# Optimization experiments

Measured on AMD Instinct MI355X. Metric: run time of the kernel, lower is better.

Reference implementation:

```python
import jax, jax.numpy as jnp
import numpy as np
from jax import lax

EPS = 1e-5
DN = ('NCHW', 'OIHW', 'NCHW')


def _bn(x, gamma, beta, mean, var):
    # eval-mode BatchNorm2d over channel dim (axis=1)
    s = gamma / jnp.sqrt(var + EPS)
    return x * s[None, :, None, None] + (beta - mean * s)[None, :, None, None]


def setup_inputs() -> dict:
    key = jax.random.key(0)
    ks = jax.random.split(key, 12)
    B, Cin, C, H, W, NC = 128, 2048, 512, 14, 14, 200
    return {
        'feature': jax.random.normal(ks[0], (B, Cin, H, W), jnp.float32),
        'w_reduce': jax.random.normal(ks[1], (C, Cin, 1, 1), jnp.float32) * 0.02,
        'b_reduce': jax.random.normal(ks[2], (C,), jnp.float32) * 0.02,
        'bn1_gamma': jnp.ones((C,), jnp.float32),
        'bn1_beta': jnp.zeros((C,), jnp.float32),
        'bn1_mean': jax.random.normal(ks[3], (C,), jnp.float32) * 0.02,
        'bn1_var': jax.random.uniform(ks[4], (C,), jnp.float32),
        'w3': jax.random.normal(ks[5], (C, C, 3, 3), jnp.float32) * 0.02,
        'b3': jax.random.normal(ks[6], (C,), jnp.float32) * 0.02,
        'bn2_gamma': jnp.ones((C,), jnp.float32),
        'bn2_beta': jnp.zeros((C,), jnp.float32),
        'bn2_mean': jax.random.normal(ks[7], (C,), jnp.float32) * 0.02,
        'bn2_var': jax.random.uniform(ks[8], (C,), jnp.float32),
        'fc1_w': jax.random.normal(ks[9], (NC, C), jnp.float32) * 0.02,
        'fc1_b': jnp.zeros((NC,), jnp.float32),
        'fc2_w': jax.random.normal(ks[10], (NC, NC), jnp.float32) * 0.02,
        'fc2_b': jnp.zeros((NC,), jnp.float32),
    }


def reference(feature, w_reduce, b_reduce, bn1_gamma, bn1_beta, bn1_mean, bn1_var,
              w3, b3, bn2_gamma, bn2_beta, bn2_mean, bn2_var,
              fc1_w, fc1_b, fc2_w, fc2_b):
    B, _, H, W = feature.shape
    C = w_reduce.shape[0]  # 512
    # reduce: 1x1 conv + BN + ReLU
    f = lax.conv_general_dilated(feature, w_reduce, (1, 1), 'VALID', dimension_numbers=DN)
    f = f + b_reduce[None, :, None, None]
    f = jax.nn.relu(_bn(f, bn1_gamma, bn1_beta, bn1_mean, bn1_var))
    x = f.reshape(B, C, H * W)  # [B, 512, 196]
    # channel affinity + softmax(-xxt) over last dim (= the per-row loop)
    xxt = jnp.einsum('bcn,bdn->bcd', x, x)  # [B, 512, 512]
    a = jax.nn.softmax(-xxt, axis=2)
    y = jnp.einsum('bcd,bdn->bcn', a, x).reshape(B, C, H, W)
    # conv3: 3x3 conv + BN + ReLU + global avg pool
    z = lax.conv_general_dilated(y, w3, (1, 1), 'SAME', dimension_numbers=DN)
    z = z + b3[None, :, None, None]
    z = jax.nn.relu(_bn(z, bn2_gamma, bn2_beta, bn2_mean, bn2_var))
    z = jnp.mean(z, axis=(2, 3))  # [B, 512]
    # fc_channel: Linear -> ReLU -> Linear
    h = jax.nn.relu(z @ fc1_w.T + fc1_b)
    sf = h @ fc2_w.T + fc2_b
    return sf
```

## Files before the change

### kernel.cpp

```cpp
#include <hip/hip_runtime.h>

typedef __attribute__((ext_vector_type(8))) short bf16x8;
typedef __attribute__((ext_vector_type(4))) float f32x4;
typedef __attribute__((ext_vector_type(4))) short short4v;

__device__ __forceinline__ unsigned short f2bf(float x){
  unsigned u = __float_as_uint(x);
  return (unsigned short)((u + 0x7FFFu + ((u>>16)&1u)) >> 16);
}
__device__ __forceinline__ float bf2f(unsigned short b){
  return __uint_as_float(((unsigned)b)<<16);
}

typedef const __attribute__((address_space(1))) void* gas_t;
typedef __attribute__((address_space(3))) void* las_t;
__device__ __forceinline__ void gl16(const void* g, void* l){
  __builtin_amdgcn_global_load_lds((gas_t)g, (las_t)l, 16, 0, 0);
}

static constexpr size_t O_FHI  = 0;
static constexpr size_t O_FLO  = 102760448;
static constexpr size_t O_XHI  = 205520896;
static constexpr size_t O_XLO  = 239075328;
static constexpr size_t O_XT   = 272629760;
static constexpr size_t O_AMAT = 301989888;
static constexpr size_t O_WH   = 369098752;
static constexpr size_t O_WL   = 371195904;
static constexpr size_t O_W3B  = 373293056;
static constexpr size_t O_PAR  = 378011648;
static constexpr size_t O_FC1T = 378019840;
static constexpr size_t O_FC2T = 378429440;
static constexpr size_t O_ZBAR = 378589440;

__global__ void k_params(const float* br, const float* g1, const float* be1, const float* m1, const float* v1,
                         const float* b3, const float* g2, const float* be2, const float* m2, const float* v2,
                         float* par){
  int c = blockIdx.x*256 + threadIdx.x;
  if (c >= 512) return;
  float s1 = g1[c] * rsqrtf(v1[c] + 1e-5f);
  par[c] = s1;
  par[512+c] = (br[c]-m1[c])*s1 + be1[c];
  float s2 = g2[c] * rsqrtf(v2[c] + 1e-5f);
  par[1024+c] = s2;
  par[1536+c] = (b3[c]-m2[c])*s2 + be2[c];
}

__global__ void k_wrhl(const float* wr, unsigned short* wh, unsigned short* wl){
  int k = blockIdx.x*256 + threadIdx.x;
  int c = blockIdx.y;
  float v = wr[(size_t)c*2048 + k];
  unsigned short h = f2bf(v);
  wh[(size_t)c*2048 + k] = h;
  wl[(size_t)c*2048 + k] = f2bf(v - bf2f(h));
}

__global__ void k_w3c(const float* w3, unsigned short* w3c){
  int k = blockIdx.x*256 + threadIdx.x;
  int co = blockIdx.y;
  int ci0b = k/576; int r2 = k - ci0b*576;
  int tap = r2>>6;  int cio = r2&63;
  w3c[(((size_t)ci0b*9 + tap)*512 + co)*64 + cio] =
      f2bf(w3[((size_t)co*512 + ci0b*64 + cio)*9 + tap]);
}

__global__ void k_fc1t(const float* w, float* wt){
  int i = blockIdx.x*256 + threadIdx.x;
  int k = i/200, j = i - k*200;
  wt[i] = w[j*512 + k];
}
__global__ void k_fc2t(const float* w, float* wt){
  int i = blockIdx.x*256 + threadIdx.x;
  if (i >= 200*200) return;
  int k = i/200, j = i - k*200;
  wt[i] = w[j*200 + k];
}

__global__ __launch_bounds__(256) void k_zeropad(unsigned short* xhi, unsigned short* xlo){
  int rr = blockIdx.x*256 + threadIdx.x;
  float4 z = {0.f,0.f,0.f,0.f};
  float4* a = (float4*)(xhi + (size_t)rr*256 + 192);
  float4* b = (float4*)(xlo + (size_t)rr*256 + 192);
  #pragma unroll
  for (int j=0;j<8;++j){ a[j] = z; b[j] = z; }
}

__global__ __launch_bounds__(256) void k_zeroyb(unsigned short* ypad){
  int tile = blockIdx.x;
  int r = threadIdx.x;
  if (r >= 256) return;
  int hi = r>>4, lo = r&15;
  bool pad = (hi==0)||(hi==15)||(lo==0)||(lo==15);
  if (!pad) return;
  float4 z = {0.f,0.f,0.f,0.f};
  float4* p = (float4*)(ypad + ((size_t)tile*256 + r)*64);
  #pragma unroll
  for (int j=0;j<8;++j) p[j] = z;
}

__global__ __launch_bounds__(256) void k_featT(const float* __restrict__ feat,
        unsigned short* __restrict__ fhi, unsigned short* __restrict__ flo){
  __shared__ float tile[64][33];
  int b = blockIdx.z;
  int ci0 = blockIdx.y*64, p0 = blockIdx.x*32;
  int t = threadIdx.x;
  int j = t & 31, i0 = t >> 5;
  for (int rep=0; rep<8; ++rep){
    int i = rep*8 + i0;
    int p = p0 + j;
    tile[i][j] = (p<196) ? feat[((size_t)b*2048 + ci0 + i)*196 + p] : 0.f;
  }
  __syncthreads();
  int ii = t & 63, jj0 = t >> 6;
  for (int rep=0; rep<8; ++rep){
    int jj = rep*4 + jj0;
    int p = p0 + jj;
    if (p < 196){
      float v = tile[ii][jj];
      unsigned short h = f2bf(v);
      size_t o = ((size_t)b*196 + p)*2048 + ci0 + ii;
      fhi[o] = h;
      flo[o] = f2bf(v - bf2f(h));
    }
  }
}

__global__ __launch_bounds__(256) void k_conv1(
    const unsigned short* __restrict__ fhi, const unsigned short* __restrict__ flo,
    const unsigned short* __restrict__ wh,  const unsigned short* __restrict__ wl,
    const float* __restrict__ par,
    unsigned short* __restrict__ xhi, unsigned short* __restrict__ xlo,
    unsigned short* __restrict__ xT){
  __shared__ char lds[32768];
  char* Als = lds; char* Bls = lds + 16384;
  int lin = blockIdx.x;
  int sz  = (lin&7)*98 + (lin>>3);
  int mt = sz&3;
  int gt = sz>>2;
  int c0 = mt*128;
  size_t g0 = (size_t)gt*128;
  int t = threadIdx.x, lane = t&63, wid = t>>6, wm = wid&1, wn = wid>>1;
  int fq = lane>>4, fr = lane&15;
  f32x4 acc[4][4] = {};
  for (int it=0; it<96; ++it){
    int seg = it>>5, kk0 = (it&31)*64;
    const unsigned short* As = (seg<2) ? wh : wl;
    const unsigned short* Bs = (seg==1) ? flo : fhi;
    __syncthreads();
    #pragma unroll
    for (int r=0;r<4;++r){
      int L = r*256 + t;
      int row = L>>3, cs = ((L&7)^(row&7))*8;
      gl16(As + (size_t)(c0+row)*2048 + kk0 + cs, Als + L*16);
      gl16(Bs + (g0+row)*2048 + kk0 + cs, Bls + L*16);
    }
    __syncthreads();
    #pragma unroll
    for (int ks=0; ks<2; ++ks){
      int kb = ks*64 + fq*16;
      bf16x8 af[4];
      #pragma unroll
      for (int m=0;m<4;++m){
        int row = wm*64 + m*16 + fr;
        af[m] = *(const bf16x8*)(Als + row*128 + (kb ^ ((row&7)<<4)));
      }
      #pragma unroll
      for (int n=0;n<4;++n){
        int row = wn*64 + n*16 + fr;
        bf16x8 bff = *(const bf16x8*)(Bls + row*128 + (kb ^ ((row&7)<<4)));
        #pragma unroll
        for (int m=0;m<4;++m)
          acc[m][n] = __builtin_amdgcn_mfma_f32_16x16x32_bf16(af[m], bff, acc[m][n],0,0,0);
      }
    }
  }
  const float* s1 = par; const float* t1 = par+512;
  for (int m=0;m<4;++m){
    int cb = c0 + wm*64 + m*16 + fq*4;
    float sc[4], sh[4];
    for (int j=0;j<4;++j){ sc[j]=s1[cb+j]; sh[j]=t1[cb+j]; }
    for (int n=0;n<4;++n){
      int gg = (int)g0 + wn*64 + n*16 + fr;
      int b = gg/196, p = gg - b*196;
      unsigned short hs[4];
      for (int j=0;j<4;++j){
        float v = fmaxf(acc[m][n][j]*sc[j]+sh[j], 0.f);
        unsigned short h = f2bf(v);
        hs[j] = h;
        size_t ic = (size_t)b*512 + cb + j;
        xhi[ic*256 + p] = h;
        xlo[ic*256 + p] = f2bf(v - bf2f(h));
      }
      *(short4v*)(xT + ((size_t)b*224 + p)*512 + cb) = *(short4v*)hs;
    }
  }
}

__global__ __launch_bounds__(256) void k_xxt(const unsigned short* __restrict__ xhi,
        const unsigned short* __restrict__ xlo, float* __restrict__ xxt){
  __shared__ char lds[32768];
  char* Als = lds; char* Bls = lds + 16384;
  int lin = blockIdx.x;
  int sz  = (lin&7)*160 + (lin>>3);
  int b = sz/10, sub = sz - b*10;
  unsigned mtp = (3u<<18)|(2u<<16)|(2u<<14)|(1u<<12)|(1u<<10)|(1u<<8)|(0u<<6)|(0u<<4)|(0u<<2)|0u;
  unsigned ntp = (3u<<18)|(3u<<16)|(2u<<14)|(3u<<12)|(2u<<10)|(1u<<8)|(3u<<6)|(2u<<4)|(1u<<2)|0u;
  int mt = (mtp>>(2*sub))&3, nt = (ntp>>(2*sub))&3;
  int c0 = mt*128, d0 = nt*128;
  int t = threadIdx.x, lane = t&63, wid = t>>6, wm = wid&1, wn = wid>>1;
  int fq = lane>>4, fr = lane&15;
  f32x4 acc[4][4] = {};
  for (int it=0; it<12; ++it){
    int seg = it>>2, kk0 = (it&3)*64;
    const unsigned short* As = (seg<2) ? xhi : xlo;
    const unsigned short* Bs = (seg==1) ? xlo : xhi;
    __syncthreads();
    #pragma unroll
    for (int r=0;r<4;++r){
      int L = r*256 + t;
      int row = L>>3, cs = ((L&7)^(row&7))*8;
      gl16(As + ((size_t)b*512 + c0 + row)*256 + kk0 + cs, Als + L*16);
      gl16(Bs + ((size_t)b*512 + d0 + row)*256 + kk0 + cs, Bls + L*16);
    }
    __syncthreads();
    #pragma unroll
    for (int ks=0; ks<2; ++ks){
      int kb = ks*64 + fq*16;
      bf16x8 af[4];
      #pragma unroll
      for (int m=0;m<4;++m){
        int row = wm*64 + m*16 + fr;
        af[m] = *(const bf16x8*)(Als + row*128 + (kb ^ ((row&7)<<4)));
      }
      #pragma unroll
      for (int n=0;n<4;++n){
        int row = wn*64 + n*16 + fr;
        bf16x8 bff = *(const bf16x8*)(Bls + row*128 + (kb ^ ((row&7)<<4)));
        #pragma unroll
        for (int m=0;m<4;++m)
          acc[m][n] = __builtin_amdgcn_mfma_f32_16x16x32_bf16(af[m], bff, acc[m][n],0,0,0);
      }
    }
  }
  for (int m=0;m<4;++m){
    int cb = c0 + wm*64 + m*16 + fq*4;
    for (int n=0;n<4;++n){
      int d = d0 + wn*64 + n*16 + fr;
      *(float4*)(xxt + ((size_t)b*512 + d)*512 + cb) = *(float4*)&acc[m][n];
    }
  }
  if (mt != nt){
    for (int m=0;m<4;++m){
      int cb = c0 + wm*64 + m*16 + fq*4;
      for (int n=0;n<4;++n){
        int d = d0 + wn*64 + n*16 + fr;
        for (int jj=0;jj<4;++jj)
          xxt[((size_t)b*512 + cb + jj)*512 + d] = acc[m][n][jj];
      }
    }
  }
}

__global__ __launch_bounds__(256) void k_softmax(const float* __restrict__ xxt, unsigned short* __restrict__ amat){
  int row = blockIdx.x*4 + (threadIdx.x>>6);
  int lane = threadIdx.x & 63;
  const float* src = xxt + (size_t)row*512 + lane*8;
  float4 v0 = *(const float4*)src;
  float4 v1 = *(const float4*)(src+4);
  float mn = fminf(fminf(fminf(v0.x,v0.y),fminf(v0.z,v0.w)),
                   fminf(fminf(v1.x,v1.y),fminf(v1.z,v1.w)));
  for (int m=32; m; m>>=1) mn = fminf(mn, __shfl_xor(mn, m, 64));
  float e[8];
  e[0]=__expf(mn-v0.x); e[1]=__expf(mn-v0.y); e[2]=__expf(mn-v0.z); e[3]=__expf(mn-v0.w);
  e[4]=__expf(mn-v1.x); e[5]=__expf(mn-v1.y); e[6]=__expf(mn-v1.z); e[7]=__expf(mn-v1.w);
  float s = e[0]+e[1]+e[2]+e[3]+e[4]+e[5]+e[6]+e[7];
  for (int m=32; m; m>>=1) s += __shfl_xor(s, m, 64);
  float inv = 1.f/s;
  short4v p0, p1;
  for (int q=0;q<4;++q) p0[q] = (short)f2bf(e[q]*inv);
  for (int q=0;q<4;++q) p1[q] = (short)f2bf(e[4+q]*inv);
  unsigned short* dst = amat + (size_t)row*512 + lane*8;
  *(short4v*)dst = p0;
  *(short4v*)(dst+4) = p1;
}

__global__ __launch_bounds__(256) void k_pv(const unsigned short* __restrict__ amat,
        const unsigned short* __restrict__ xT, unsigned short* __restrict__ ypad){
  __shared__ char lds[30720];
  char* Als = lds; char* Bls = lds + 16384;
  int lin = blockIdx.x, per = gridDim.x>>3;
  int sz  = (lin&7)*per + (lin>>3);
  int b = sz>>3, sub = sz&7, mt = sub>>1, nt = sub&1;
  int c0 = mt*128, n0 = nt*112;
  int t = threadIdx.x, lane = t&63, wid = t>>6;
  int fq = lane>>4, fr = lane&15;
  f32x4 acc[2][7] = {};
  for (int it=0; it<8; ++it){
    int k0 = it*64;
    __syncthreads();
    #pragma unroll
    for (int r=0;r<4;++r){
      int L = r*256 + t;
      int row = L>>3, cs = ((L&7)^(row&7))*8;
      gl16(amat + ((size_t)b*512 + c0 + row)*512 + k0 + cs, Als + L*16);
    }
    #pragma unroll
    for (int r=0;r<4;++r){
      int L = r*256 + t;
      if (L < 896){
        int row = L>>3, cs = ((L&7)^(row&7))*8;
        gl16(xT + ((size_t)b*224 + n0 + row)*512 + k0 + cs, Bls + L*16);
      }
    }
    __syncthreads();
    #pragma unroll
    for (int ks=0; ks<2; ++ks){
      int kb = ks*64 + fq*16;
      bf16x8 af[2];
      #pragma unroll
      for (int m=0;m<2;++m){
        int row = wid*32 + m*16 + fr;
        af[m] = *(const bf16x8*)(Als + row*128 + (kb ^ ((row&7)<<4)));
      }
      #pragma unroll
      for (int n=0;n<7;++n){
        int row = n*16 + fr;
        bf16x8 bff = *(const bf16x8*)(Bls + row*128 + (kb ^ ((row&7)<<4)));
        #pragma unroll
        for (int m=0;m<2;++m)
          acc[m][n] = __builtin_amdgcn_mfma_f32_16x16x32_bf16(af[m], bff, acc[m][n],0,0,0);
      }
    }
  }
  for (int m=0;m<2;++m){
    int cb = c0 + wid*32 + m*16 + fq*4;
    int ci0b = cb>>6, cio = cb&63;
    for (int n=0;n<7;++n){
      int p = n0 + n*16 + fr;
      if (p < 196){
        int hh = p/14, wwp = p - hh*14;
        int prow = (hh+1)*16 + (wwp+1);
        short4v pk;
        for (int j=0;j<4;++j) pk[j] = (short)f2bf(acc[m][n][j]);
        *(short4v*)(ypad + (((size_t)b*8 + ci0b)*256 + prow)*64 + cio) = pk;
      }
    }
  }
}

__global__ __launch_bounds__(512, 4) void k_conv3(const unsigned short* __restrict__ ypad,
        const unsigned short* __restrict__ w3c, const float* __restrict__ par,
        float* __restrict__ zbar){
  __shared__ char lds[65536];
  char* WIN = lds;
  char* AB0 = lds + 32768;
  char* AB1 = lds + 49152;
  int bx = blockIdx.x;
  int xcd = bx&7, jj2 = bx>>3;
  int b = xcd*16 + (jj2>>2), cot = jj2&3;
  int c0 = cot*128;
  int t = threadIdx.x, lane = t&63, w = t>>6;
  int wm = w>>1, wn = w&1;
  int fq = lane>>4, fr = lane&15;
  int frB = (fr<14) ? fr : 13;
  bool pok = (fr<14);
  f32x4 acc[2][7] = {};
  for (int ci0=0; ci0<8; ++ci0){
    const unsigned short* wsrc = ypad + ((size_t)(b*8 + ci0)*256)*64;
    #pragma unroll
    for (int r=0;r<4;++r){
      int L = r*512 + t;
      int row = L>>3, cs = ((L&7)^(row&7))*8;
      gl16(wsrc + row*64 + cs, WIN + L*16);
    }
    {
      const unsigned short* asrc = w3c + ((size_t)(ci0*9 + 0)*512 + c0)*64;
      #pragma unroll
      for (int r=0;r<2;++r){
        int L = r*512 + t;
        int row = L>>3, cs = ((L&7)^(row&7))*8;
        gl16(asrc + row*64 + cs, AB0 + L*16);
      }
    }
    __syncthreads();
    for (int tap=0; tap<9; ++tap){
      char* Acur = (tap&1) ? AB1 : AB0;
      char* Anxt = (tap&1) ? AB0 : AB1;
      if (tap < 8){
        const unsigned short* asrc = w3c + ((size_t)(ci0*9 + tap+1)*512 + c0)*64;
        #pragma unroll
        for (int r=0;r<2;++r){
          int L = r*512 + t;
          int row = L>>3, cs = ((L&7)^(row&7))*8;
          gl16(asrc + row*64 + cs, Anxt + L*16);
        }
      }
      int kh = tap/3, kw = tap - kh*3;
      bf16x8 ah[2][2];
      #pragma unroll
      for (int ks=0;ks<2;++ks)
        #pragma unroll
        for (int m=0;m<2;++m){
          int row = wm*32 + m*16 + fr;
          ah[ks][m] = *(const bf16x8*)(Acur + row*128 + (((ks*4+fq)^(row&7))<<4));
        }
      int col = frB + kw;
      __builtin_amdgcn_s_setprio(1);
      #pragma unroll
      for (int n=0;n<7;++n){
        int prow = (wn*7 + n + kh)*16 + col;
        #pragma unroll
        for (int ks=0;ks<2;++ks){
          bf16x8 bf = *(const bf16x8*)(WIN + prow*128 + (((ks*4+fq)^(prow&7))<<4));
          acc[0][n] = __builtin_amdgcn_mfma_f32_16x16x32_bf16(ah[ks][0], bf, acc[0][n],0,0,0);
          acc[1][n] = __builtin_amdgcn_mfma_f32_16x16x32_bf16(ah[ks][1], bf, acc[1][n],0,0,0);
        }
      }
      __builtin_amdgcn_s_setprio(0);
      __syncthreads();
    }
  }
  const float* s2 = par+1024; const float* t2 = par+1536;
  float ps[2][4];
  #pragma unroll
  for (int m=0;m<2;++m){
    int cb = c0 + wm*32 + m*16 + fq*4;
    #pragma unroll
    for (int j=0;j<4;++j){
      float sc = s2[cb+j], sh = t2[cb+j];
      float s = 0.f;
      #pragma unroll
      for (int n=0;n<7;++n)
        s += fmaxf(acc[m][n][j]*sc + sh, 0.f);
      ps[m][j] = pok ? s : 0.f;
    }
  }
  #pragma unroll
  for (int off=1; off<16; off<<=1)
    #pragma unroll
    for (int m=0;m<2;++m)
      #pragma unroll
      for (int j=0;j<4;++j)
        ps[m][j] += __shfl_xor(ps[m][j], off, 64);
  float* part = (float*)lds;
  if (fr == 0){
    #pragma unroll
    for (int m=0;m<2;++m)
      #pragma unroll
      for (int j=0;j<4;++j)
        part[wn*128 + wm*32 + m*16 + fq*4 + j] = ps[m][j];
  }
  __syncthreads();
  if (t < 128)
    zbar[(size_t)b*512 + c0 + t] = part[t] + part[128 + t];
}

__global__ __launch_bounds__(256) void k_fc(const float* __restrict__ zbar,
        const float* __restrict__ fc1T, const float* __restrict__ fc1b,
        const float* __restrict__ fc2T, const float* __restrict__ fc2b,
        float* __restrict__ out){
  __shared__ float zb[512];
  __shared__ float hl[200];
  int b = blockIdx.x, t = threadIdx.x;
  zb[t]     = zbar[(size_t)b*512 + t]       * (1.f/196.f);
  zb[t+256] = zbar[(size_t)b*512 + t + 256] * (1.f/196.f);
  __syncthreads();
  if (t < 200){
    float acc = fc1b[t];
    for (int k=0;k<512;++k) acc += zb[k]*fc1T[k*200+t];
    hl[t] = fmaxf(acc, 0.f);
  }
  __syncthreads();
  if (t < 200){
    float acc = fc2b[t];
    for (int k=0;k<200;++k) acc += hl[k]*fc2T[k*200+t];
    out[(size_t)b*200 + t] = acc;
  }
}

extern "C" void kernel_launch(void* const* d_in, const int* in_sizes, int n_in,
                              void* d_out, int out_size, void* d_ws, size_t ws_size,
                              hipStream_t stream) {
  const float* feature  = (const float*)d_in[0];
  const float* w_reduce = (const float*)d_in[1];
  const float* b_reduce = (const float*)d_in[2];
  const float* g1  = (const float*)d_in[3];
  const float* be1 = (const float*)d_in[4];
  const float* m1  = (const float*)d_in[5];
  const float* v1  = (const float*)d_in[6];
  const float* w3  = (const float*)d_in[7];
  const float* b3  = (const float*)d_in[8];
  const float* g2  = (const float*)d_in[9];
  const float* be2 = (const float*)d_in[10];
  const float* m2  = (const float*)d_in[11];
  const float* v2  = (const float*)d_in[12];
  const float* fc1w = (const float*)d_in[13];
  const float* fc1b = (const float*)d_in[14];
  const float* fc2w = (const float*)d_in[15];
  const float* fc2b = (const float*)d_in[16];

  char* ws = (char*)d_ws;
  unsigned short* fhi  = (unsigned short*)(ws + O_FHI);
  unsigned short* flo  = (unsigned short*)(ws + O_FLO);
  float*          xxt  = (float*)(ws + O_FHI);
  unsigned short* xhi  = (unsigned short*)(ws + O_XHI);
  unsigned short* xlo  = (unsigned short*)(ws + O_XLO);
  unsigned short* ypad = (unsigned short*)(ws + O_XLO);
  unsigned short* xT   = (unsigned short*)(ws + O_XT);
  unsigned short* amat = (unsigned short*)(ws + O_AMAT);
  unsigned short* wh   = (unsigned short*)(ws + O_WH);
  unsigned short* wl   = (unsigned short*)(ws + O_WL);
  unsigned short* w3c  = (unsigned short*)(ws + O_W3B);
  float* par  = (float*)(ws + O_PAR);
  float* fc1T = (float*)(ws + O_FC1T);
  float* fc2T = (float*)(ws + O_FC2T);
  float* zbar = (float*)(ws + O_ZBAR);

  k_params<<<2, 256, 0, stream>>>(b_reduce, g1, be1, m1, v1, b3, g2, be2, m2, v2, par);
  k_wrhl<<<dim3(8,512), 256, 0, stream>>>(w_reduce, wh, wl);
  k_w3c<<<dim3(18,512), 256, 0, stream>>>(w3, w3c);
  k_fc1t<<<400, 256, 0, stream>>>(fc1w, fc1T);
  k_fc2t<<<157, 256, 0, stream>>>(fc2w, fc2T);
  k_zeropad<<<256, 256, 0, stream>>>(xhi, xlo);

  k_featT<<<dim3(7,32,128), 256, 0, stream>>>(feature, fhi, flo);
  k_conv1<<<784, 256, 0, stream>>>(fhi, flo, wh, wl, par, xhi, xlo, xT);

  k_xxt<<<1280, 256, 0, stream>>>(xhi, xlo, xxt);
  k_softmax<<<16384, 256, 0, stream>>>(xxt, amat);

  k_zeroyb<<<1024, 256, 0, stream>>>(ypad);
  k_pv<<<1024, 256, 0, stream>>>(amat, xT, ypad);
  k_conv3<<<512, 512, 0, stream>>>(ypad, w3c, par, zbar);
  k_fc<<<128, 256, 0, stream>>>(zbar, fc1T, fc1b, fc2T, fc2b, (float*)d_out);
}
```

Before: 686.1 us.

## Pipeline conv1 with triple-buffered LDS, merge prep kernels, fold padding zeroing

Conv1 moves to 128x256 tiles with a three-stage global_load_lds pipeline. The split-bf16 products (hi*hi, hi*lo, lo*hi) are now computed in one pass over K instead of three sequential K sweeps. The six small preprocessing kernels are merged into one launch, the ypad border zeroing moves into k_pv, and featT writes packed pairs. This cuts launch overhead and load latency stalls, but a single 144KB-LDS block per CU lowers occupancy and adds register pressure.

New measurement: 660.4 us. 3.7% less time.

```diff
diff --git a/kernel.cpp b/kernel.cpp
--- a/kernel.cpp
+++ b/kernel.cpp
@@ -3,6 +3,7 @@
 typedef __attribute__((ext_vector_type(8))) short bf16x8;
 typedef __attribute__((ext_vector_type(4))) float f32x4;
 typedef __attribute__((ext_vector_type(4))) short short4v;
+typedef __attribute__((ext_vector_type(2))) short short2v;
 
 __device__ __forceinline__ unsigned short f2bf(float x){
   unsigned u = __float_as_uint(x);
@@ -32,69 +33,50 @@
 static constexpr size_t O_FC2T = 378429440;
 static constexpr size_t O_ZBAR = 378589440;
 
-__global__ void k_params(const float* br, const float* g1, const float* be1, const float* m1, const float* v1,
-                         const float* b3, const float* g2, const float* be2, const float* m2, const float* v2,
-                         float* par){
-  int c = blockIdx.x*256 + threadIdx.x;
-  if (c >= 512) return;
-  float s1 = g1[c] * rsqrtf(v1[c] + 1e-5f);
-  par[c] = s1;
-  par[512+c] = (br[c]-m1[c])*s1 + be1[c];
-  float s2 = g2[c] * rsqrtf(v2[c] + 1e-5f);
-  par[1024+c] = s2;
-  par[1536+c] = (b3[c]-m2[c])*s2 + be2[c];
-}
-
-__global__ void k_wrhl(const float* wr, unsigned short* wh, unsigned short* wl){
-  int k = blockIdx.x*256 + threadIdx.x;
-  int c = blockIdx.y;
-  float v = wr[(size_t)c*2048 + k];
-  unsigned short h = f2bf(v);
-  wh[(size_t)c*2048 + k] = h;
-  wl[(size_t)c*2048 + k] = f2bf(v - bf2f(h));
-}
-
-__global__ void k_w3c(const float* w3, unsigned short* w3c){
-  int k = blockIdx.x*256 + threadIdx.x;
-  int co = blockIdx.y;
-  int ci0b = k/576; int r2 = k - ci0b*576;
-  int tap = r2>>6;  int cio = r2&63;
-  w3c[(((size_t)ci0b*9 + tap)*512 + co)*64 + cio] =
-      f2bf(w3[((size_t)co*512 + ci0b*64 + cio)*9 + tap]);
-}
-
-__global__ void k_fc1t(const float* w, float* wt){
-  int i = blockIdx.x*256 + threadIdx.x;
-  int k = i/200, j = i - k*200;
-  wt[i] = w[j*512 + k];
-}
-__global__ void k_fc2t(const float* w, float* wt){
-  int i = blockIdx.x*256 + threadIdx.x;
-  if (i >= 200*200) return;
-  int k = i/200, j = i - k*200;
-  wt[i] = w[j*200 + k];
-}
-
-__global__ __launch_bounds__(256) void k_zeropad(unsigned short* xhi, unsigned short* xlo){
-  int rr = blockIdx.x*256 + threadIdx.x;
-  float4 z = {0.f,0.f,0.f,0.f};
-  float4* a = (float4*)(xhi + (size_t)rr*256 + 192);
-  float4* b = (float4*)(xlo + (size_t)rr*256 + 192);
-  #pragma unroll
-  for (int j=0;j<8;++j){ a[j] = z; b[j] = z; }
-}
-
-__global__ __launch_bounds__(256) void k_zeroyb(unsigned short* ypad){
-  int tile = blockIdx.x;
-  int r = threadIdx.x;
-  if (r >= 256) return;
-  int hi = r>>4, lo = r&15;
-  bool pad = (hi==0)||(hi==15)||(lo==0)||(lo==15);
-  if (!pad) return;
-  float4 z = {0.f,0.f,0.f,0.f};
-  float4* p = (float4*)(ypad + ((size_t)tile*256 + r)*64);
-  #pragma unroll
-  for (int j=0;j<8;++j) p[j] = z;
+__global__ __launch_bounds__(256) void k_prep(
+    const float* wr, unsigned short* wh, unsigned short* wl,
+    const float* w3, unsigned short* w3c,
+    const float* fc1w, float* fc1T, const float* fc2w, float* fc2T,
+    const float* br, const float* g1, const float* be1, const float* m1, const float* v1,
+    const float* b3, const float* g2, const float* be2, const float* m2, const float* v2,
+    float* par, unsigned short* xhi, unsigned short* xlo){
+  int blk = blockIdx.x, t = threadIdx.x;
+  if (blk < 4096){
+    int idx = blk*256 + t;
+    int c = idx >> 11, k = idx & 2047;
+    float v = wr[(size_t)c*2048 + k];
+    unsigned short h = f2bf(v);
+    wh[(size_t)c*2048+k] = h; wl[(size_t)c*2048+k] = f2bf(v - bf2f(h));
+  } else if (blk < 13312){
+    int i = (blk-4096)*256 + t;
+    int co = i / 4608, k = i - co*4608;
+    int ci0b = k / 576, r2 = k - ci0b*576;
+    int tap = r2 >> 6, cio = r2 & 63;
+    w3c[(((size_t)ci0b*9+tap)*512+co)*64+cio] =
+        f2bf(w3[((size_t)co*512 + ci0b*64+cio)*9 + tap]);
+  } else if (blk < 13712){
+    int i = (blk-13312)*256 + t;
+    int k = i/200, j = i - k*200;
+    fc1T[i] = fc1w[j*512+k];
+  } else if (blk < 13869){
+    int i = (blk-13712)*256 + t;
+    if (i < 40000){ int k = i/200, j = i - k*200; fc2T[i] = fc2w[j*200+k]; }
+  } else if (blk < 13871){
+    int c = (blk-13869)*256 + t;
+    if (c < 512){
+      float s1 = g1[c]*rsqrtf(v1[c]+1e-5f);
+      par[c] = s1; par[512+c] = (br[c]-m1[c])*s1 + be1[c];
+      float s2 = g2[c]*rsqrtf(v2[c]+1e-5f);
+      par[1024+c] = s2; par[1536+c] = (b3[c]-m2[c])*s2 + be2[c];
+    }
+  } else {
+    int rr = (blk-13871)*256 + t;
+    float4 z = {0.f,0.f,0.f,0.f};
+    float4* a = (float4*)(xhi + (size_t)rr*256 + 192);
+    float4* bq = (float4*)(xlo + (size_t)rr*256 + 192);
+    #pragma unroll
+    for (int q=0;q<8;++q){ a[q]=z; bq[q]=z; }
+  }
 }
 
 __global__ __launch_bounds__(256) void k_featT(const float* __restrict__ feat,
@@ -110,76 +92,110 @@
     tile[i][j] = (p<196) ? feat[((size_t)b*2048 + ci0 + i)*196 + p] : 0.f;
   }
   __syncthreads();
-  int ii = t & 63, jj0 = t >> 6;
-  for (int rep=0; rep<8; ++rep){
-    int jj = rep*4 + jj0;
+  int j2 = t & 31;
+  int jj0 = t >> 5;
+  for (int rep=0; rep<4; ++rep){
+    int jj = rep*8 + jj0;
     int p = p0 + jj;
     if (p < 196){
-      float v = tile[ii][jj];
-      unsigned short h = f2bf(v);
-      size_t o = ((size_t)b*196 + p)*2048 + ci0 + ii;
-      fhi[o] = h;
-      flo[o] = f2bf(v - bf2f(h));
-    }
-  }
-}
-
-__global__ __launch_bounds__(256) void k_conv1(
+      float v0 = tile[2*j2][jj], v1 = tile[2*j2+1][jj];
+      unsigned short h0 = f2bf(v0), h1 = f2bf(v1);
+      unsigned short l0 = f2bf(v0 - bf2f(h0)), l1 = f2bf(v1 - bf2f(h1));
+      size_t o = ((size_t)b*196 + p)*2048 + ci0 + 2*j2;
+      short2v hv; hv[0]=(short)h0; hv[1]=(short)h1;
+      short2v lv; lv[0]=(short)l0; lv[1]=(short)l1;
+      *(short2v*)(fhi + o) = hv;
+      *(short2v*)(flo + o) = lv;
+    }
+  }
+}
+
+__global__ __launch_bounds__(256, 1) void k_conv1(
     const unsigned short* __restrict__ fhi, const unsigned short* __restrict__ flo,
     const unsigned short* __restrict__ wh,  const unsigned short* __restrict__ wl,
     const float* __restrict__ par,
     unsigned short* __restrict__ xhi, unsigned short* __restrict__ xlo,
     unsigned short* __restrict__ xT){
-  __shared__ char lds[32768];
-  char* Als = lds; char* Bls = lds + 16384;
+  __shared__ char lds[147456];
   int lin = blockIdx.x;
-  int sz  = (lin&7)*98 + (lin>>3);
+  int sz  = (lin&7)*49 + (lin>>3);
   int mt = sz&3;
   int gt = sz>>2;
   int c0 = mt*128;
-  size_t g0 = (size_t)gt*128;
-  int t = threadIdx.x, lane = t&63, wid = t>>6, wm = wid&1, wn = wid>>1;
-  int fq = lane>>4, fr = lane&15;
-  f32x4 acc[4][4] = {};
-  for (int it=0; it<96; ++it){
-    int seg = it>>5, kk0 = (it&31)*64;
-    const unsigned short* As = (seg<2) ? wh : wl;
-    const unsigned short* Bs = (seg==1) ? flo : fhi;
-    __syncthreads();
-    #pragma unroll
-    for (int r=0;r<4;++r){
-      int L = r*256 + t;
-      int row = L>>3, cs = ((L&7)^(row&7))*8;
-      gl16(As + (size_t)(c0+row)*2048 + kk0 + cs, Als + L*16);
-      gl16(Bs + (g0+row)*2048 + kk0 + cs, Bls + L*16);
-    }
-    __syncthreads();
-    #pragma unroll
-    for (int ks=0; ks<2; ++ks){
-      int kb = ks*64 + fq*16;
-      bf16x8 af[4];
-      #pragma unroll
-      for (int m=0;m<4;++m){
-        int row = wm*64 + m*16 + fr;
-        af[m] = *(const bf16x8*)(Als + row*128 + (kb ^ ((row&7)<<4)));
-      }
+  size_t g0 = (size_t)gt*256;
+  int t = threadIdx.x, lane = t&63, wv = t>>6;
+  int fq = (lane>>4)&3, fr = lane&15;
+  f32x4 acc[8][4] = {};
+
+  auto STAGE = [&](int it, char* buf){
+    #pragma unroll
+    for (int jj=0; jj<12; ++jj){
+      const unsigned short* src; int ldsoff;
+      if (jj < 4){
+        int g = (jj&1)*256 + t;
+        int row = g>>2;
+        int cs = ((g&3) ^ ((row>>1)&3))*8;
+        src = ((jj<2)? wh : wl) + (size_t)(c0+row)*2048 + it*32 + cs;
+        ldsoff = ((jj<2)? 0 : 8192) + g*16;
+      } else {
+        int g = (jj&3)*256 + t;
+        int row = g>>2;
+        int cs = ((g&3) ^ ((row>>1)&3))*8;
+        src = ((jj<8)? fhi : flo) + (g0+row)*2048 + it*32 + cs;
+        ldsoff = ((jj<8)? 16384 : 32768) + g*16;
+      }
+      gl16(src, buf + ldsoff);
+    }
+  };
+
+  char* b0 = lds;
+  char* b1 = lds + 49152;
+  char* b2 = lds + 98304;
+  STAGE(0, b0);
+  STAGE(1, b1);
+
+  for (int it=0; it<64; ++it){
+    if (it < 63) { asm volatile("s_waitcnt vmcnt(12)" ::: "memory"); }
+    else         { asm volatile("s_waitcnt vmcnt(0)"  ::: "memory"); }
+    __builtin_amdgcn_s_barrier();
+    __builtin_amdgcn_sched_barrier(0);
+    if (it+2 < 64) STAGE(it+2, b2);
+    {
+      const char* A = b0; const char* B = b0 + 16384;
+      bf16x8 ah[8], al[8];
+      #pragma unroll
+      for (int m=0;m<8;++m){
+        int row = m*16 + fr;
+        int off = row*64 + ((fq*16) ^ (((row>>1)&3)<<4));
+        ah[m] = *(const bf16x8*)(A + off);
+        al[m] = *(const bf16x8*)(A + 8192 + off);
+      }
+      __builtin_amdgcn_s_setprio(1);
       #pragma unroll
       for (int n=0;n<4;++n){
-        int row = wn*64 + n*16 + fr;
-        bf16x8 bff = *(const bf16x8*)(Bls + row*128 + (kb ^ ((row&7)<<4)));
+        int row = wv*64 + n*16 + fr;
+        int off = row*64 + ((fq*16) ^ (((row>>1)&3)<<4));
+        bf16x8 bh = *(const bf16x8*)(B + off);
+        bf16x8 bl = *(const bf16x8*)(B + 16384 + off);
         #pragma unroll
-        for (int m=0;m<4;++m)
-          acc[m][n] = __builtin_amdgcn_mfma_f32_16x16x32_bf16(af[m], bff, acc[m][n],0,0,0);
-      }
-    }
-  }
+        for (int m=0;m<8;++m){
+          acc[m][n] = __builtin_amdgcn_mfma_f32_16x16x32_bf16(ah[m], bh, acc[m][n],0,0,0);
+          acc[m][n] = __builtin_amdgcn_mfma_f32_16x16x32_bf16(ah[m], bl, acc[m][n],0,0,0);
+          acc[m][n] = __builtin_amdgcn_mfma_f32_16x16x32_bf16(al[m], bh, acc[m][n],0,0,0);
+        }
+      }
+      __builtin_amdgcn_s_setprio(0);
+    }
+    char* tmp = b0; b0 = b1; b1 = b2; b2 = tmp;
+  }
+
   const float* s1 = par; const float* t1 = par+512;
-  for (int m=0;m<4;++m){
-    int cb = c0 + wm*64 + m*16 + fq*4;
+  for (int m=0;m<8;++m){
+    int cb = c0 + m*16 + fq*4;
     float sc[4], sh[4];
     for (int j=0;j<4;++j){ sc[j]=s1[cb+j]; sh[j]=t1[cb+j]; }
     for (int n=0;n<4;++n){
-      int gg = (int)g0 + wn*64 + n*16 + fr;
+      int gg = (int)g0 + wv*64 + n*16 + fr;
       int b = gg/196, p = gg - b*196;
       unsigned short hs[4];
       for (int j=0;j<4;++j){
@@ -293,6 +309,16 @@
   int c0 = mt*128, n0 = nt*112;
   int t = threadIdx.x, lane = t&63, wid = t>>6;
   int fq = lane>>4, fr = lane&15;
+  {
+    int r = t;
+    int hi = r>>4, lo2 = r&15;
+    if (hi==0||hi==15||lo2==0||lo2==15){
+      float4 z = {0.f,0.f,0.f,0.f};
+      float4* pz = (float4*)(ypad + (((size_t)b*8 + sub)*256 + r)*64);
+      #pragma unroll
+      for (int q=0;q<8;++q) pz[q] = z;
+    }
+  }
   f32x4 acc[2][7] = {};
   for (int it=0; it<8; ++it){
     int k0 = it*64;
@@ -515,20 +541,16 @@
   float* fc2T = (float*)(ws + O_FC2T);
   float* zbar = (float*)(ws + O_ZBAR);
 
-  k_params<<<2, 256, 0, stream>>>(b_reduce, g1, be1, m1, v1, b3, g2, be2, m2, v2, par);
-  k_wrhl<<<dim3(8,512), 256, 0, stream>>>(w_reduce, wh, wl);
-  k_w3c<<<dim3(18,512), 256, 0, stream>>>(w3, w3c);
-  k_fc1t<<<400, 256, 0, stream>>>(fc1w, fc1T);
-  k_fc2t<<<157, 256, 0, stream>>>(fc2w, fc2T);
-  k_zeropad<<<256, 256, 0, stream>>>(xhi, xlo);
+  k_prep<<<14127, 256, 0, stream>>>(w_reduce, wh, wl, w3, w3c,
+      fc1w, fc1T, fc2w, fc2T,
+      b_reduce, g1, be1, m1, v1, b3, g2, be2, m2, v2, par, xhi, xlo);
 
   k_featT<<<dim3(7,32,128), 256, 0, stream>>>(feature, fhi, flo);
-  k_conv1<<<784, 256, 0, stream>>>(fhi, flo, wh, wl, par, xhi, xlo, xT);
+  k_conv1<<<392, 256, 0, stream>>>(fhi, flo, wh, wl, par, xhi, xlo, xT);
 
   k_xxt<<<1280, 256, 0, stream>>>(xhi, xlo, xxt);
   k_softmax<<<16384, 256, 0, stream>>>(xxt, amat);
 
-  k_zeroyb<<<1024, 256, 0, stream>>>(ypad);
   k_pv<<<1024, 256, 0, stream>>>(amat, xT, ypad);
   k_conv3<<<512, 512, 0, stream>>>(ypad, w3c, par, zbar);
   k_fc<<<128, 256, 0, stream>>>(zbar, fc1T, fc1b, fc2T, fc2b, (float*)d_out);
```
